# Performance work log

Hardware: AMD Instinct MI355X
Metric: run time of the kernel (lower is better)

## Reference

```python
import jax, jax.numpy as jnp
import numpy as np

D_MODEL = 1024
N_HEADS = 16
D_HEAD = D_MODEL // N_HEADS
WINDOW = 256
DILATION = 1
GLOBAL_IDX = (0,)
NEG_INF = float('-inf')


def longformer_mask(seq_len):
    # Vectorized version of the original O(S^2) Python-loop mask builder.
    i = jnp.arange(seq_len)[:, None]
    j = jnp.arange(seq_len)[None, :]
    d = jnp.abs(i - j)
    window_ok = (d <= WINDOW) & (d % DILATION == 0)  # includes diagonal (d==0)
    is_global = jnp.zeros((seq_len,), dtype=bool).at[jnp.array(GLOBAL_IDX)].set(True)
    global_ok = is_global[:, None] | is_global[None, :]
    return jnp.where(window_ok | global_ok, 0.0, NEG_INF).astype(jnp.float32)


def setup_inputs() -> dict:
    key = jax.random.key(0)
    ks = jax.random.split(key, 9)
    s = 1.0 / np.sqrt(D_MODEL)
    inp = {'x': jax.random.normal(ks[0], (2, 2048, D_MODEL), dtype=jnp.float32)}
    for n, kw, kb in (('q', ks[1], ks[2]), ('k', ks[3], ks[4]), ('v', ks[5], ks[6]), ('o', ks[7], ks[8])):
        inp['W' + n] = jax.random.uniform(kw, (D_MODEL, D_MODEL), jnp.float32, -s, s)
        inp['b' + n] = jax.random.uniform(kb, (D_MODEL,), jnp.float32, -s, s)
    return inp


def reference(x, Wq, bq, Wk, bk, Wv, bv, Wo, bo):
    B, S, _ = x.shape
    scale = D_HEAD ** -0.5

    def split_heads(t):  # [B,S,D] -> [B,H,S,d]
        return t.reshape(B, S, N_HEADS, D_HEAD).transpose(0, 2, 1, 3)

    Q = split_heads(x @ Wq + bq)
    K = split_heads(x @ Wk + bk)
    V = split_heads(x @ Wv + bv)

    scores = jnp.einsum('bhqd,bhkd->bhqk', Q, K) * scale
    scores = scores + longformer_mask(S)[None, None]
    attn = jax.nn.softmax(scores, axis=-1)  # dropout is identity in eval
    out = jnp.einsum('bhqk,bhkd->bhqd', attn, V)
    out = out.transpose(0, 2, 1, 3).reshape(B, S, D_MODEL)
    return out @ Wo + bo
```

## Files before the change

### kernel.cpp

```cpp
#include <hip/hip_runtime.h>
#include <hip/hip_bf16.h>

typedef __attribute__((ext_vector_type(8))) short short8;
typedef __attribute__((ext_vector_type(4))) float floatx4;
typedef __attribute__((ext_vector_type(8))) _Float16 half8;
typedef __attribute__((ext_vector_type(4))) _Float16 half4;

using bf16 = __hip_bfloat16;
using fp16 = _Float16;

#define S_LEN 2048
#define DM 1024
#define NH 16
#define DH 64
#define WIN 256

__device__ __forceinline__ unsigned short f2b(float f) {
  __hip_bfloat16 h = __float2bfloat16(f);
  return *reinterpret_cast<unsigned short*>(&h);
}
__device__ __forceinline__ unsigned short f2h(float f) {
  fp16 h = (fp16)f;
  return *reinterpret_cast<unsigned short*>(&h);
}
__device__ __forceinline__ void lds_load16(void* lds, const void* gptr) {
  __builtin_amdgcn_global_load_lds(
      (const __attribute__((address_space(1))) unsigned int*)gptr,
      (__attribute__((address_space(3))) unsigned int*)lds, 16, 0, 0);
}

__global__ __launch_bounds__(256) void k_convert_x(const float4* __restrict__ in,
                                                   ushort4* __restrict__ out) {
  int i = blockIdx.x * 256 + threadIdx.x;
  float4 v = in[i];
  ushort4 r;
  r.x = f2b(v.x); r.y = f2b(v.y); r.z = f2b(v.z); r.w = f2b(v.w);
  out[i] = r;
}

__global__ __launch_bounds__(256) void k_transpose_cvt(const float* __restrict__ W0,
                                                       const float* __restrict__ W1,
                                                       const float* __restrict__ W2,
                                                       const float* __restrict__ W3,
                                                       bf16* __restrict__ out) {
  __shared__ float t[32][33];
  const float* W = (blockIdx.z == 0) ? W0 : (blockIdx.z == 1) ? W1 : (blockIdx.z == 2) ? W2 : W3;
  bf16* O = out + (size_t)blockIdx.z * 1024 * 1024;
  int x0 = blockIdx.x * 32, y0 = blockIdx.y * 32;
  int tx = threadIdx.x, ty = threadIdx.y;
  #pragma unroll
  for (int i = 0; i < 32; i += 8) t[ty + i][tx] = W[(size_t)(y0 + ty + i) * 1024 + x0 + tx];
  __syncthreads();
  #pragma unroll
  for (int i = 0; i < 32; i += 8)
    O[(size_t)(x0 + ty + i) * 1024 + y0 + tx] = __float2bfloat16(t[tx][ty + i]);
}

template <int MODE>
__global__ __launch_bounds__(256) void k_gemm(const bf16* __restrict__ A,
                                              const bf16* __restrict__ Bt,
                                              const float* __restrict__ bias_q,
                                              const float* __restrict__ bias_k,
                                              const float* __restrict__ bias_v,
                                              fp16* __restrict__ Qh, fp16* __restrict__ Kh,
                                              fp16* __restrict__ Vt, float* __restrict__ outF) {
  __shared__ __align__(16) bf16 As[128 * 32];
  __shared__ __align__(16) bf16 Bs[128 * 32];
  const int tid = threadIdx.x;
  const int wave = tid >> 6, lane = tid & 63;
  const int m0 = blockIdx.y * 128, n0 = blockIdx.x * 128;
  const int r0 = tid >> 2;
  const int cb = (tid & 3) * 16;
  const char* Ag = (const char*)A + (size_t)(m0 + r0) * 2048 + cb;
  const char* Bg = (const char*)Bt + (size_t)(n0 + r0) * 2048 + cb;
  char* AsW0 = (char*)As + wave * 1024;
  char* AsW1 = (char*)As + 4096 + wave * 1024;
  char* BsW0 = (char*)Bs + wave * 1024;
  char* BsW1 = (char*)Bs + 4096 + wave * 1024;
  const int wm = (wave & 1) * 64, wn = (wave >> 1) * 64;
  const int ln = lane & 15, quad = lane >> 4;

  floatx4 acc[4][4];
  #pragma unroll
  for (int i = 0; i < 4; i++)
    #pragma unroll
    for (int j = 0; j < 4; j++) acc[i][j] = (floatx4){0.f, 0.f, 0.f, 0.f};

  for (int k0 = 0; k0 < 1024; k0 += 32) {
    __syncthreads();
    lds_load16(AsW0, Ag + k0 * 2);
    lds_load16(AsW1, Ag + 64 * 2048 + k0 * 2);
    lds_load16(BsW0, Bg + k0 * 2);
    lds_load16(BsW1, Bg + 64 * 2048 + k0 * 2);
    __syncthreads();
    short8 af[4], bfr[4];
    #pragma unroll
    for (int mi = 0; mi < 4; mi++)
      af[mi] = *(const short8*)&As[(wm + mi * 16 + ln) * 32 + quad * 8];
    #pragma unroll
    for (int ni = 0; ni < 4; ni++)
      bfr[ni] = *(const short8*)&Bs[(wn + ni * 16 + ln) * 32 + quad * 8];
    #pragma unroll
    for (int mi = 0; mi < 4; mi++)
      #pragma unroll
      for (int ni = 0; ni < 4; ni++)
        acc[mi][ni] = __builtin_amdgcn_mfma_f32_16x16x32_bf16(af[mi], bfr[ni], acc[mi][ni], 0, 0, 0);
  }

  if constexpr (MODE == 0) {
    #pragma unroll
    for (int ni = 0; ni < 4; ni++) {
      int n = n0 + wn + ni * 16 + ln;
      int g = n >> 10, nn = n & 1023;
      int h = nn >> 6, dd = nn & 63;
      if (g == 2) {
        float bias = bias_v[nn];
        #pragma unroll
        for (int mi = 0; mi < 4; mi++) {
          int m = m0 + wm + mi * 16 + quad * 4;
          int b = m >> 11, s = m & 2047;
          ushort4 pk;
          pk.x = f2h(acc[mi][ni][0] + bias);
          pk.y = f2h(acc[mi][ni][1] + bias);
          pk.z = f2h(acc[mi][ni][2] + bias);
          pk.w = f2h(acc[mi][ni][3] + bias);
          *(ushort4*)&Vt[((size_t)(b * NH + h) * DH + dd) * S_LEN + s] = pk;
        }
      } else {
        const float* bp = (g == 0) ? bias_q : bias_k;
        fp16* og = (g == 0) ? Qh : Kh;
        float bias = bp[nn];
        #pragma unroll
        for (int mi = 0; mi < 4; mi++) {
          #pragma unroll
          for (int r = 0; r < 4; r++) {
            int m = m0 + wm + mi * 16 + quad * 4 + r;
            int b = m >> 11, s = m & 2047;
            og[(size_t)((b * NH + h) * S_LEN + s) * DH + dd] = (fp16)(acc[mi][ni][r] + bias);
          }
        }
      }
    }
  } else {
    #pragma unroll
    for (int ni = 0; ni < 4; ni++) {
      int n = n0 + wn + ni * 16 + ln;
      float bias = bias_q[n];
      #pragma unroll
      for (int mi = 0; mi < 4; mi++)
        #pragma unroll
        for (int r = 0; r < 4; r++) {
          int m = m0 + wm + mi * 16 + quad * 4 + r;
          outF[(size_t)m * 1024 + n] = acc[mi][ni][r] + bias;
        }
    }
  }
}

__global__ __launch_bounds__(256, 4) void k_attn(const fp16* __restrict__ Qh,
                                                 const fp16* __restrict__ Kh,
                                                 const fp16* __restrict__ Vt,
                                                 bf16* __restrict__ aout) {
  __shared__ __align__(16) fp16 KsL[2][64 * 72];
  __shared__ __align__(16) fp16 VsL[2][64 * 72];

  const int i = blockIdx.x;
  const int xcd = i & 7, rr = i >> 3;
  const int bh = xcd * 4 + (rr & 3);
  const int tile = rr >> 2;
  const int b = bh >> 4, h = bh & 15;
  const size_t base = (size_t)bh * S_LEN * DH;
  const fp16* Qp = Qh + base;
  const fp16* Kp = Kh + base;
  const fp16* Vp = Vt + base;
  const float SC2 = 0.18033688011112042f;
  const int tid = threadIdx.x;

  if (tile == 32) {
    float* sP = (float*)&KsL[0][0];
    float* oR = (float*)&VsL[0][0];
    float* red = (float*)&VsL[1][0];
    const int wv = tid >> 6, lane = tid & 63;
    const int g = lane >> 3, e8 = lane & 7;
    const half8 q0t = *(const half8*)(Qp + e8 * 8);
    float lsum = 0.f;
    for (int it = 0; it < 64; ++it) {
      int grp = wv * 64 + it;
      const half8 kv = *(const half8*)(Kp + (size_t)(grp * 8 + g) * DH + e8 * 8);
      float p = 0.f;
      #pragma unroll
      for (int e = 0; e < 8; ++e) p += (float)q0t[e] * (float)kv[e];
      p += __shfl_xor(p, 1, 64);
      p += __shfl_xor(p, 2, 64);
      p += __shfl_xor(p, 4, 64);
      p = exp2f(fmaf(p, SC2, -8.f));
      if (e8 == 0) sP[grp * 8 + g] = p;
      lsum += p;
    }
    #pragma unroll
    for (int off = 1; off < 64; off <<= 1) lsum += __shfl_xor(lsum, off, 64);
    if (lane == 0) red[wv] = lsum;
    __syncthreads();
    const float ltot = (red[0] + red[1] + red[2] + red[3]) * 0.125f;
    const int d = tid & 63, qu = tid >> 6;
    float o = 0.f;
    for (int j0 = qu * 512; j0 < qu * 512 + 512; j0 += 8) {
      half8 vv = *(const half8*)(Vp + (size_t)d * S_LEN + j0);
      #pragma unroll
      for (int e = 0; e < 8; ++e) o += sP[j0 + e] * (float)vv[e];
    }
    oR[tid] = o;
    __syncthreads();
    if (tid < 64) {
      float oo = oR[tid] + oR[tid + 64] + oR[tid + 128] + oR[tid + 192];
      aout[(size_t)(b * S_LEN) * DM + h * DH + tid] = __float2bfloat16(oo / ltot);
    }
    return;
  }

  const int w = tid >> 6, lane = tid & 63;
  const int ln = lane & 15, quad = lane >> 4;
  const int qb = tile * 64;
  const int qw = qb + w * 16;

  const half8 bq0 = *(const half8*)(Qp + (size_t)(qw + ln) * DH + quad * 8);
  const half8 bq1 = *(const half8*)(Qp + (size_t)(qw + ln) * DH + 32 + quad * 8);

  floatx4 acc[4];
  float l_i;

  {
    const half8 k0a = *(const half8*)(Kp + quad * 8);
    const half8 k0b = *(const half8*)(Kp + 32 + quad * 8);
    float s0 = 0.f;
    #pragma unroll
    for (int e = 0; e < 8; ++e)
      s0 += (float)bq0[e] * (float)k0a[e] + (float)bq1[e] * (float)k0b[e];
    s0 += __shfl_xor(s0, 16, 64);
    s0 += __shfl_xor(s0, 32, 64);
    float p0 = exp2f(fmaf(s0, SC2, -8.f));
    l_i = (quad == 0) ? p0 : 0.f;
    #pragma unroll
    for (int dt = 0; dt < 4; ++dt)
      #pragma unroll
      for (int r = 0; r < 4; ++r)
        acc[dt][r] = p0 * (float)Vp[(size_t)(dt * 16 + quad * 4 + r) * S_LEN];
  }

  int cs = qb - WIN; if (cs < 0) cs = 0;
  int ce = qb + 64 + WIN; if (ce > S_LEN) ce = S_LEN;

  const int f0 = tid, f1 = tid + 256;
  const int r0s = f0 >> 3, c0s = (f0 & 7) * 8;
  const int r1s = f1 >> 3, c1s = (f1 & 7) * 8;

  uint4 kreg0, kreg1, vreg0, vreg1;
  auto stage_load = [&](int c) {
    kreg0 = *(const uint4*)(Kp + (size_t)(c + r0s) * DH + c0s);
    kreg1 = *(const uint4*)(Kp + (size_t)(c + r1s) * DH + c1s);
    vreg0 = *(const uint4*)(Vp + (size_t)r0s * S_LEN + c + c0s);
    vreg1 = *(const uint4*)(Vp + (size_t)r1s * S_LEN + c + c1s);
  };
  auto stage_write = [&](int buf) {
    *(uint4*)&KsL[buf][r0s * 72 + c0s] = kreg0;
    *(uint4*)&KsL[buf][r1s * 72 + c1s] = kreg1;
    *(uint4*)&VsL[buf][r0s * 72 + c0s] = vreg0;
    *(uint4*)&VsL[buf][r1s * 72 + c1s] = vreg1;
  };

  auto compute = [&](int c, int buf) {
    floatx4 s[4];
    #pragma unroll
    for (int jt = 0; jt < 4; ++jt) {
      half8 k0 = *(const half8*)&KsL[buf][(jt * 16 + ln) * 72 + quad * 8];
      half8 k1 = *(const half8*)&KsL[buf][(jt * 16 + ln) * 72 + 32 + quad * 8];
      floatx4 z = (floatx4){0.f, 0.f, 0.f, 0.f};
      z = __builtin_amdgcn_mfma_f32_16x16x32_f16(k0, bq0, z, 0, 0, 0);
      s[jt] = __builtin_amdgcn_mfma_f32_16x16x32_f16(k1, bq1, z, 0, 0, 0);
    }
    half4 v01[8];
    #pragma unroll
    for (int dt = 0; dt < 2; ++dt)
      #pragma unroll
      for (int jt = 0; jt < 4; ++jt)
        v01[dt * 4 + jt] =
            *(const half4*)&VsL[buf][(dt * 16 + ln) * 72 + jt * 16 + quad * 4];
    const bool full_in = (c != 0) && (c >= qw - 241) && (c <= qw + 193);
    half4 Pt[4];
    if (full_in) {
      #pragma unroll
      for (int jt = 0; jt < 4; ++jt)
        #pragma unroll
        for (int r = 0; r < 4; ++r) {
          float pe = exp2f(fmaf(s[jt][r], SC2, -8.f));
          Pt[jt][r] = (fp16)pe;
          l_i += pe;
        }
    } else {
      const int q = qw + ln;
      #pragma unroll
      for (int jt = 0; jt < 4; ++jt) {
        #pragma unroll
        for (int r = 0; r < 4; ++r) {
          int j = c + jt * 16 + quad * 4 + r;
          int dq = q - j;
          bool ok = (dq <= WIN && dq >= -WIN) && (j != 0);
          float pe = ok ? exp2f(fmaf(s[jt][r], SC2, -8.f)) : 0.f;
          Pt[jt][r] = (fp16)pe;
          l_i += pe;
        }
      }
    }
    half4 v23[8];
    #pragma unroll
    for (int dt = 0; dt < 2; ++dt)
      #pragma unroll
      for (int jt = 0; jt < 4; ++jt)
        v23[dt * 4 + jt] =
            *(const half4*)&VsL[buf][((dt + 2) * 16 + ln) * 72 + jt * 16 + quad * 4];
    #pragma unroll
    for (int jt = 0; jt < 4; ++jt) {
      acc[0] = __builtin_amdgcn_mfma_f32_16x16x16f16(v01[jt], Pt[jt], acc[0], 0, 0, 0);
      acc[1] = __builtin_amdgcn_mfma_f32_16x16x16f16(v01[4 + jt], Pt[jt], acc[1], 0, 0, 0);
    }
    #pragma unroll
    for (int jt = 0; jt < 4; ++jt) {
      acc[2] = __builtin_amdgcn_mfma_f32_16x16x16f16(v23[jt], Pt[jt], acc[2], 0, 0, 0);
      acc[3] = __builtin_amdgcn_mfma_f32_16x16x16f16(v23[4 + jt], Pt[jt], acc[3], 0, 0, 0);
    }
  };

  stage_load(cs);
  stage_write(0);
  __syncthreads();
  int buf = 0;
  for (int c = cs; c < ce; c += 64) {
    const bool hasnext = (c + 64 < ce);
    if (hasnext) stage_load(c + 64);
    compute(c, buf);
    if (hasnext) stage_write(buf ^ 1);
    __syncthreads();
    buf ^= 1;
  }

  float lt = l_i;
  lt += __shfl_xor(lt, 16, 64);
  lt += __shfl_xor(lt, 32, 64);
  const float inv = 1.0f / lt;
  const int q = qw + ln;
  if (q != 0) {
    #pragma unroll
    for (int dt = 0; dt < 4; ++dt) {
      ushort4 pk;
      pk.x = f2b(acc[dt][0] * inv);
      pk.y = f2b(acc[dt][1] * inv);
      pk.z = f2b(acc[dt][2] * inv);
      pk.w = f2b(acc[dt][3] * inv);
      *(ushort4*)&aout[(size_t)(b * S_LEN + q) * DM + h * DH + dt * 16 + quad * 4] = pk;
    }
  }
}

extern "C" void kernel_launch(void* const* d_in, const int* in_sizes, int n_in,
                              void* d_out, int out_size, void* d_ws, size_t ws_size,
                              hipStream_t stream) {
  const float* x  = (const float*)d_in[0];
  const float* Wq = (const float*)d_in[1];
  const float* bq = (const float*)d_in[2];
  const float* Wk = (const float*)d_in[3];
  const float* bk = (const float*)d_in[4];
  const float* Wv = (const float*)d_in[5];
  const float* bv = (const float*)d_in[6];
  const float* Wo = (const float*)d_in[7];
  const float* bo = (const float*)d_in[8];
  float* out = (float*)d_out;

  const size_t SEG = (size_t)4096 * 1024;
  bf16* xb = (bf16*)d_ws;
  bf16* wT = xb + SEG;
  fp16* Qh = (fp16*)(wT + SEG);
  fp16* Kh = Qh + SEG;
  fp16* Vt = Kh + SEG;
  bf16* ao = (bf16*)(Vt + SEG);

  k_convert_x<<<dim3(4096), dim3(256), 0, stream>>>((const float4*)x, (ushort4*)xb);
  k_transpose_cvt<<<dim3(32, 32, 4), dim3(32, 8), 0, stream>>>(Wq, Wk, Wv, Wo, wT);
  k_gemm<0><<<dim3(24, 32), dim3(256), 0, stream>>>(xb, wT, bq, bk, bv, Qh, Kh, Vt, nullptr);
  k_attn<<<dim3(1056), dim3(256), 0, stream>>>(Qh, Kh, Vt, ao);
  k_gemm<1><<<dim3(8, 32), dim3(256), 0, stream>>>(ao, wT + (size_t)3 * 1024 * 1024, bo,
                                                   nullptr, nullptr, nullptr, nullptr, nullptr, out);
}
```

Measured before the change: 207.9 us.

## Merge prep kernels, double GEMM k-step, and remap GEMM blocks per XCD

The x conversion and weight transpose/convert kernels are merged into one launch, with a fifth z-slice handling x. The GEMM now loads two 32-wide k slices per barrier pair, halving the number of syncs per K loop and issuing more MFMAs between them. GEMM block indices are remapped so that blocks landing on the same XCD share row tiles of A, aiming for better L2 reuse. These changes cost extra LDS and registers per block, which may lower occupancy.

```diff
diff --git a/kernel.cpp b/kernel.cpp
--- a/kernel.cpp
+++ b/kernel.cpp
@@ -29,25 +29,32 @@
       (__attribute__((address_space(3))) unsigned int*)lds, 16, 0, 0);
 }
 
-__global__ __launch_bounds__(256) void k_convert_x(const float4* __restrict__ in,
-                                                   ushort4* __restrict__ out) {
-  int i = blockIdx.x * 256 + threadIdx.x;
-  float4 v = in[i];
-  ushort4 r;
-  r.x = f2b(v.x); r.y = f2b(v.y); r.z = f2b(v.z); r.w = f2b(v.w);
-  out[i] = r;
-}
-
-__global__ __launch_bounds__(256) void k_transpose_cvt(const float* __restrict__ W0,
-                                                       const float* __restrict__ W1,
-                                                       const float* __restrict__ W2,
-                                                       const float* __restrict__ W3,
-                                                       bf16* __restrict__ out) {
+__global__ __launch_bounds__(256) void k_prep(const float* __restrict__ x,
+                                              const float* __restrict__ W0,
+                                              const float* __restrict__ W1,
+                                              const float* __restrict__ W2,
+                                              const float* __restrict__ W3,
+                                              bf16* __restrict__ wT,
+                                              ushort4* __restrict__ xb) {
+  const int tx = threadIdx.x, ty = threadIdx.y;
+  if (blockIdx.z == 4) {
+    const int tid = ty * 32 + tx;
+    const int blk = blockIdx.y * 32 + blockIdx.x;
+    const float4* in4 = (const float4*)x;
+    #pragma unroll
+    for (int k = 0; k < 4; ++k) {
+      int i = k * 262144 + blk * 256 + tid;
+      float4 v = in4[i];
+      ushort4 o;
+      o.x = f2b(v.x); o.y = f2b(v.y); o.z = f2b(v.z); o.w = f2b(v.w);
+      xb[i] = o;
+    }
+    return;
+  }
   __shared__ float t[32][33];
   const float* W = (blockIdx.z == 0) ? W0 : (blockIdx.z == 1) ? W1 : (blockIdx.z == 2) ? W2 : W3;
-  bf16* O = out + (size_t)blockIdx.z * 1024 * 1024;
+  bf16* O = wT + (size_t)blockIdx.z * 1024 * 1024;
   int x0 = blockIdx.x * 32, y0 = blockIdx.y * 32;
-  int tx = threadIdx.x, ty = threadIdx.y;
   #pragma unroll
   for (int i = 0; i < 32; i += 8) t[ty + i][tx] = W[(size_t)(y0 + ty + i) * 1024 + x0 + tx];
   __syncthreads();
@@ -64,19 +71,22 @@
                                               const float* __restrict__ bias_v,
                                               fp16* __restrict__ Qh, fp16* __restrict__ Kh,
                                               fp16* __restrict__ Vt, float* __restrict__ outF) {
-  __shared__ __align__(16) bf16 As[128 * 32];
-  __shared__ __align__(16) bf16 Bs[128 * 32];
+  __shared__ __align__(16) bf16 As[2][128 * 32];
+  __shared__ __align__(16) bf16 Bs[2][128 * 32];
   const int tid = threadIdx.x;
   const int wave = tid >> 6, lane = tid & 63;
-  const int m0 = blockIdx.y * 128, n0 = blockIdx.x * 128;
+  const int gi = blockIdx.x;
+  const int xcd = gi & 7, grr = gi >> 3;
+  const int m0 = (xcd * 4 + (grr & 3)) * 128;
+  const int n0 = (grr >> 2) * 128;
   const int r0 = tid >> 2;
   const int cb = (tid & 3) * 16;
   const char* Ag = (const char*)A + (size_t)(m0 + r0) * 2048 + cb;
   const char* Bg = (const char*)Bt + (size_t)(n0 + r0) * 2048 + cb;
-  char* AsW0 = (char*)As + wave * 1024;
-  char* AsW1 = (char*)As + 4096 + wave * 1024;
-  char* BsW0 = (char*)Bs + wave * 1024;
-  char* BsW1 = (char*)Bs + 4096 + wave * 1024;
+  char* As0W = (char*)&As[0][0] + wave * 1024;
+  char* As1W = (char*)&As[1][0] + wave * 1024;
+  char* Bs0W = (char*)&Bs[0][0] + wave * 1024;
+  char* Bs1W = (char*)&Bs[1][0] + wave * 1024;
   const int wm = (wave & 1) * 64, wn = (wave >> 1) * 64;
   const int ln = lane & 15, quad = lane >> 4;
 
@@ -86,25 +96,35 @@
     #pragma unroll
     for (int j = 0; j < 4; j++) acc[i][j] = (floatx4){0.f, 0.f, 0.f, 0.f};
 
-  for (int k0 = 0; k0 < 1024; k0 += 32) {
+  for (int k0 = 0; k0 < 1024; k0 += 64) {
     __syncthreads();
-    lds_load16(AsW0, Ag + k0 * 2);
-    lds_load16(AsW1, Ag + 64 * 2048 + k0 * 2);
-    lds_load16(BsW0, Bg + k0 * 2);
-    lds_load16(BsW1, Bg + 64 * 2048 + k0 * 2);
+    lds_load16(As0W,        Ag + k0 * 2);
+    lds_load16(As0W + 4096, Ag + 64 * 2048 + k0 * 2);
+    lds_load16(As1W,        Ag + k0 * 2 + 64);
+    lds_load16(As1W + 4096, Ag + 64 * 2048 + k0 * 2 + 64);
+    lds_load16(Bs0W,        Bg + k0 * 2);
+    lds_load16(Bs0W + 4096, Bg + 64 * 2048 + k0 * 2);
+    lds_load16(Bs1W,        Bg + k0 * 2 + 64);
+    lds_load16(Bs1W + 4096, Bg + 64 * 2048 + k0 * 2 + 64);
     __syncthreads();
-    short8 af[4], bfr[4];
+    short8 af0[4], af1[4], bf0[4], bf1[4];
+    #pragma unroll
+    for (int mi = 0; mi < 4; mi++) {
+      af0[mi] = *(const short8*)&As[0][(wm + mi * 16 + ln) * 32 + quad * 8];
+      af1[mi] = *(const short8*)&As[1][(wm + mi * 16 + ln) * 32 + quad * 8];
+    }
+    #pragma unroll
+    for (int ni = 0; ni < 4; ni++) {
+      bf0[ni] = *(const short8*)&Bs[0][(wn + ni * 16 + ln) * 32 + quad * 8];
+      bf1[ni] = *(const short8*)&Bs[1][(wn + ni * 16 + ln) * 32 + quad * 8];
+    }
     #pragma unroll
     for (int mi = 0; mi < 4; mi++)
-      af[mi] = *(const short8*)&As[(wm + mi * 16 + ln) * 32 + quad * 8];
-    #pragma unroll
-    for (int ni = 0; ni < 4; ni++)
-      bfr[ni] = *(const short8*)&Bs[(wn + ni * 16 + ln) * 32 + quad * 8];
-    #pragma unroll
-    for (int mi = 0; mi < 4; mi++)
-      #pragma unroll
-      for (int ni = 0; ni < 4; ni++)
-        acc[mi][ni] = __builtin_amdgcn_mfma_f32_16x16x32_bf16(af[mi], bfr[ni], acc[mi][ni], 0, 0, 0);
+      #pragma unroll
+      for (int ni = 0; ni < 4; ni++) {
+        acc[mi][ni] = __builtin_amdgcn_mfma_f32_16x16x32_bf16(af0[mi], bf0[ni], acc[mi][ni], 0, 0, 0);
+        acc[mi][ni] = __builtin_amdgcn_mfma_f32_16x16x32_bf16(af1[mi], bf1[ni], acc[mi][ni], 0, 0, 0);
+      }
   }
 
   if constexpr (MODE == 0) {
@@ -383,10 +403,9 @@
   fp16* Vt = Kh + SEG;
   bf16* ao = (bf16*)(Vt + SEG);
 
-  k_convert_x<<<dim3(4096), dim3(256), 0, stream>>>((const float4*)x, (ushort4*)xb);
-  k_transpose_cvt<<<dim3(32, 32, 4), dim3(32, 8), 0, stream>>>(Wq, Wk, Wv, Wo, wT);
-  k_gemm<0><<<dim3(24, 32), dim3(256), 0, stream>>>(xb, wT, bq, bk, bv, Qh, Kh, Vt, nullptr);
+  k_prep<<<dim3(32, 32, 5), dim3(32, 8), 0, stream>>>(x, Wq, Wk, Wv, Wo, wT, (ushort4*)xb);
+  k_gemm<0><<<dim3(768), dim3(256), 0, stream>>>(xb, wT, bq, bk, bv, Qh, Kh, Vt, nullptr);
   k_attn<<<dim3(1056), dim3(256), 0, stream>>>(Qh, Kh, Vt, ao);
-  k_gemm<1><<<dim3(8, 32), dim3(256), 0, stream>>>(ao, wT + (size_t)3 * 1024 * 1024, bo,
-                                                   nullptr, nullptr, nullptr, nullptr, nullptr, out);
-}
+  k_gemm<1><<<dim3(256), dim3(256), 0, stream>>>(ao, wT + (size_t)3 * 1024 * 1024, bo,
+                                                 nullptr, nullptr, nullptr, nullptr, nullptr, out);
+}
```

Result: faster. 195.8 us (-5.8%).
